# Performance work log

Measured on AMD Instinct MI355X. Metric: run time of the kernel, lower is better.

## Reference

```python
import jax, jax.numpy as jnp
import numpy as np

EPS = 1e-8  # torch CosineSimilarity default eps

def _normalize(x):
    # torch clamps each norm at eps before dividing
    n = jnp.sqrt(jnp.sum(x * x, axis=-1, keepdims=True))
    return x / jnp.maximum(n, EPS)

def _cross_entropy(logits, labels):
    logp = jax.nn.log_softmax(logits, axis=-1)
    return -jnp.mean(jnp.take_along_axis(logp, labels[:, None], axis=-1))

def setup_inputs() -> dict:
    key = jax.random.key(0)
    ks = jax.random.split(key, 7)
    B, M, D = 8192, 3129, 512
    return {
        'mm_proj': jax.random.normal(ks[0], (B, D), jnp.float32),
        'ans_embedding': jax.random.normal(ks[1], (M, D), jnp.float32),
        'v_max': jax.random.normal(ks[2], (B, D), jnp.float32),
        'mm': jax.random.normal(ks[3], (B, D), jnp.float32),
        'logits_q': jax.random.normal(ks[4], (B, M), jnp.float32),
        'logits_rubi': jax.random.normal(ks[5], (B, M), jnp.float32),
        'class_id': jax.random.randint(ks[6], (B, 1), 0, M, jnp.int64),
    }

def reference(mm_proj, ans_embedding, v_max, mm, logits_q, logits_rubi, class_id,
              question_loss_weight=1.0):
    cid = class_id.squeeze(1)  # [B]
    # NCE over cosine similarities: fuse normalize + GEMM instead of [B,M,D] expand
    g = _normalize(mm_proj)          # [B, D]
    a = _normalize(ans_embedding)    # [M, D]
    d_logit = jnp.einsum('bd,md->bm', g, a)  # [B, M] cosine matrix
    positive_dist = jnp.take_along_axis(d_logit, cid[:, None], axis=1)[:, 0]  # [B]
    num = jnp.exp(positive_dist)
    den = jnp.sum(jnp.exp(d_logit), axis=-1)
    loss_nce = jnp.mean(-jnp.log(num / den))
    # object cosine loss
    obj_dist = jnp.sum(_normalize(v_max) * _normalize(mm), axis=-1)  # [B]
    obj_loss = jnp.mean(1.0 - obj_dist)
    fusion_loss = (_cross_entropy(logits_rubi, cid) + obj_loss + loss_nce) / 3.0
    question_loss = _cross_entropy(logits_q, cid)
    loss = fusion_loss + question_loss_weight * question_loss
    # out['loss'], out['loss_mm_q'], out['loss_q']
    return jnp.stack([loss, fusion_loss, question_loss])
```

## Files before the change

### kernel.cpp

```cpp
#include <hip/hip_runtime.h>
#include <hip/hip_bf16.h>

#define B_N 8192
#define M_N 3129
#define M_PAD 3200
#define D_N 512

#define CE_L 12
#define CE_SPAN (CE_L * 256)
#define CE_WPA 8344
#define CE_WTOT (2 * CE_WPA)
#define CE_BLOCKS (CE_WTOT / 4)

#define PREP_G_BLOCKS   (B_N / 4)
#define PREP_A_BLOCKS   (M_PAD / 4)
#define PREP_OBJ_BLOCKS (B_N / 4)
#define ZERO_FLOATS (3 * B_N + 8)
#define ZERO_BLOCKS 25
#define A_BLOCKS (PREP_G_BLOCKS + PREP_A_BLOCKS + PREP_OBJ_BLOCKS + ZERO_BLOCKS)

#define GEMM_TILES ((M_PAD / 128) * (B_N / 128))
#define B_BLOCKS 8000
#define POS_BLOCKS_B (B_BLOCKS - GEMM_TILES - CE_BLOCKS)

#define GLOBAL_AS __attribute__((address_space(1)))
#define LDS_AS __attribute__((address_space(3)))

typedef __bf16 bf16x8 __attribute__((ext_vector_type(8)));
typedef float f32x4 __attribute__((ext_vector_type(4)));

__device__ __forceinline__ f32x4 nt_load4(const float* p) {
  return __builtin_nontemporal_load((const f32x4*)p);
}

__device__ __forceinline__ void ce_span(
    int gw, const float* __restrict__ lq, const float* __restrict__ lr,
    float* __restrict__ rowsum) {
  const int lane = threadIdx.x & 63;
  const int aidx = (gw >= CE_WPA) ? 1 : 0;
  const unsigned wl = (unsigned)(gw - aidx * CE_WPA);
  const unsigned f0 = wl * (unsigned)CE_SPAN;
  const unsigned r0 = f0 / (unsigned)M_N;
  const unsigned b1 = (r0 + 1u) * (unsigned)M_N;
  const float* base = aidx ? lr : lq;
  const float* p = base + f0 + (unsigned)lane * 4u;

  f32x4 buf[6];
#pragma unroll
  for (int i = 0; i < 6; ++i) buf[i] = nt_load4(p + i * 256);

  float a0 = 0.f, a1 = 0.f;
  const unsigned fbase = f0 + (unsigned)lane * 4u;
#pragma unroll
  for (int i = 0; i < CE_L; ++i) {
    f32x4 v = buf[i % 6];
    if (i + 6 < CE_L) buf[i % 6] = nt_load4(p + (i + 6) * 256);
    unsigned f = fbase + (unsigned)i * 256u;
    float e0 = __expf(v.x), e1 = __expf(v.y), e2 = __expf(v.z), e3 = __expf(v.w);
    float lo = 0.f, hi = 0.f;
    if (f + 0u < b1) lo += e0; else hi += e0;
    if (f + 1u < b1) lo += e1; else hi += e1;
    if (f + 2u < b1) lo += e2; else hi += e2;
    if (f + 3u < b1) lo += e3; else hi += e3;
    a0 += lo; a1 += hi;
  }
  for (int o = 1; o < 64; o <<= 1) {
    a0 += __shfl_xor(a0, o);
    a1 += __shfl_xor(a1, o);
  }
  if (lane == 0) {
    float* rs = rowsum + (aidx ? B_N : 0);
    atomicAdd(rs + r0, a0);
    if (a1 != 0.f) atomicAdd(rs + r0 + 1, a1);
  }
}

__device__ __forceinline__ void normalize_row(
    const float* __restrict__ x, __bf16* __restrict__ y,
    int row, int nrows_src, int lane) {
  bf16x8 out;
  if (row >= nrows_src) {
    for (int j = 0; j < 8; ++j) out[j] = (__bf16)0.0f;
    *(bf16x8*)(y + (size_t)row * D_N + lane * 8) = out;
    return;
  }
  const float* xr = x + (size_t)row * D_N + lane * 8;
  f32x4 v0 = *(const f32x4*)xr;
  f32x4 v1 = *(const f32x4*)(xr + 4);
  float s = v0.x*v0.x + v0.y*v0.y + v0.z*v0.z + v0.w*v0.w
          + v1.x*v1.x + v1.y*v1.y + v1.z*v1.z + v1.w*v1.w;
  for (int o = 1; o < 64; o <<= 1) s += __shfl_xor(s, o);
  float rn = 1.0f / fmaxf(sqrtf(s), 1e-8f);
  float vals[8] = {v0.x, v0.y, v0.z, v0.w, v1.x, v1.y, v1.z, v1.w};
  for (int j = 0; j < 8; ++j) out[j] = (__bf16)(vals[j] * rn);
  *(bf16x8*)(y + (size_t)row * D_N + lane * 8) = out;
}

__global__ __launch_bounds__(256) void a_prep_kernel(
    const float* __restrict__ mm_proj, const float* __restrict__ ans_emb,
    const float* __restrict__ v_max, const float* __restrict__ mm,
    __bf16* __restrict__ g, __bf16* __restrict__ a,
    float* __restrict__ obj, float* __restrict__ zbase) {
  int blk = blockIdx.x;
  int wid = threadIdx.x >> 6, lane = threadIdx.x & 63;
  if (blk < PREP_G_BLOCKS) {
    normalize_row(mm_proj, g, blk * 4 + wid, B_N, lane);
  } else if (blk < PREP_G_BLOCKS + PREP_A_BLOCKS) {
    normalize_row(ans_emb, a, (blk - PREP_G_BLOCKS) * 4 + wid, M_N, lane);
  } else if (blk < PREP_G_BLOCKS + PREP_A_BLOCKS + PREP_OBJ_BLOCKS) {
    int b = (blk - PREP_G_BLOCKS - PREP_A_BLOCKS) * 4 + wid;
    const float* vr = v_max + (size_t)b * D_N + lane * 8;
    const float* mr = mm + (size_t)b * D_N + lane * 8;
    f32x4 a0 = nt_load4(vr), a1 = nt_load4(vr + 4);
    f32x4 b0 = nt_load4(mr), b1 = nt_load4(mr + 4);
    float sv = a0.x*a0.x + a0.y*a0.y + a0.z*a0.z + a0.w*a0.w
             + a1.x*a1.x + a1.y*a1.y + a1.z*a1.z + a1.w*a1.w;
    float sm = b0.x*b0.x + b0.y*b0.y + b0.z*b0.z + b0.w*b0.w
             + b1.x*b1.x + b1.y*b1.y + b1.z*b1.z + b1.w*b1.w;
    float sd = a0.x*b0.x + a0.y*b0.y + a0.z*b0.z + a0.w*b0.w
             + a1.x*b1.x + a1.y*b1.y + a1.z*b1.z + a1.w*b1.w;
    for (int o = 1; o < 64; o <<= 1) {
      sv += __shfl_xor(sv, o);
      sm += __shfl_xor(sm, o);
      sd += __shfl_xor(sd, o);
    }
    if (lane == 0) {
      float dist = sd / (fmaxf(sqrtf(sv), 1e-8f) * fmaxf(sqrtf(sm), 1e-8f));
      obj[b] = 1.0f - dist;
    }
  } else {
    int zb = blk - (PREP_G_BLOCKS + PREP_A_BLOCKS + PREP_OBJ_BLOCKS);
    int idx = (zb * 256 + threadIdx.x) * 4;
    if (idx < ZERO_FLOATS) *(f32x4*)(zbase + idx) = f32x4{0.f, 0.f, 0.f, 0.f};
  }
}

__device__ __forceinline__ void gemm_stage(
    const __bf16* __restrict__ g, const __bf16* __restrict__ a,
    __bf16* As, __bf16* Bs, int t, int brow0, int mrow0, int k0) {
#pragma unroll
  for (int i = 0; i < 2; ++i) {
    int s = t + i * 256;
    int row = s >> 2;
    int kq = (s & 3) << 3;
    const __bf16* ga = g + (size_t)(brow0 + row) * D_N + (k0 + kq);
    __builtin_amdgcn_global_load_lds((const GLOBAL_AS void*)ga,
                                     (LDS_AS void*)(As + s * 8), 16, 0, 0);
    const __bf16* gb = a + (size_t)(mrow0 + row) * D_N + (k0 + kq);
    __builtin_amdgcn_global_load_lds((const GLOBAL_AS void*)gb,
                                     (LDS_AS void*)(Bs + s * 8), 16, 0, 0);
  }
}

__global__ __launch_bounds__(256) void b_fused_kernel(
    const __bf16* __restrict__ g, const __bf16* __restrict__ a,
    const int* __restrict__ cid,
    const float* __restrict__ mm_proj, const float* __restrict__ ans_emb,
    const float* __restrict__ lq, const float* __restrict__ lr,
    float* __restrict__ den, float* __restrict__ pos,
    float* __restrict__ rowsum) {
  __shared__ __bf16 As[2][128 * 32];
  __shared__ __bf16 Bs[2][128 * 32];
  const int t = threadIdx.x;
  const int lane = t & 63;
  const int wid = t >> 6;

  const int blk = blockIdx.x;
  const int mod = blk % 5;
  const int div5 = blk / 5;

  if (mod == 2) {
    const int tile = div5;
    const int brow0 = (tile / (M_PAD / 128)) * 128;
    const int mrow0 = (tile % (M_PAD / 128)) * 128;
    const int wrow = wid >> 1;
    const int wcol = wid & 1;
    const int r = lane & 15;
    const int quad = lane >> 4;

    f32x4 acc[4][4];
    for (int i = 0; i < 4; ++i)
      for (int j = 0; j < 4; ++j)
        acc[i][j] = f32x4{0.f, 0.f, 0.f, 0.f};

    gemm_stage(g, a, &As[0][0], &Bs[0][0], t, brow0, mrow0, 0);
    int cur = 0;
    __syncthreads();

    for (int ks = 0; ks < D_N / 32; ++ks) {
      if (ks + 1 < D_N / 32)
        gemm_stage(g, a, &As[cur ^ 1][0], &Bs[cur ^ 1][0], t, brow0, mrow0,
                   (ks + 1) * 32);
      bf16x8 af[4], bfr[4];
#pragma unroll
      for (int i = 0; i < 4; ++i)
        af[i] = *(const bf16x8*)(&As[cur][(wrow * 64 + i * 16 + r) * 32 + quad * 8]);
#pragma unroll
      for (int j = 0; j < 4; ++j)
        bfr[j] = *(const bf16x8*)(&Bs[cur][(wcol * 64 + j * 16 + r) * 32 + quad * 8]);
#pragma unroll
      for (int i = 0; i < 4; ++i)
#pragma unroll
        for (int j = 0; j < 4; ++j)
          acc[i][j] = __builtin_amdgcn_mfma_f32_16x16x32_bf16(af[i], bfr[j],
                                                              acc[i][j], 0, 0, 0);
      __syncthreads();
      cur ^= 1;
    }

    for (int i = 0; i < 4; ++i) {
      for (int reg = 0; reg < 4; ++reg) {
        float s = 0.0f;
        for (int j = 0; j < 4; ++j) {
          int m = mrow0 + wcol * 64 + j * 16 + r;
          if (m < M_N) s += __expf(acc[i][j][reg]);
        }
        s += __shfl_xor(s, 1);
        s += __shfl_xor(s, 2);
        s += __shfl_xor(s, 4);
        s += __shfl_xor(s, 8);
        if (r == 0) {
          int b = brow0 + wrow * 64 + i * 16 + quad * 4 + reg;
          atomicAdd(den + b, s);
        }
      }
    }
    return;
  }

  const int other = div5 * 4 + mod - (mod > 2 ? 1 : 0);
  if (other < CE_BLOCKS) {
    ce_span(other * 4 + wid, lq, lr, rowsum);
    return;
  }

  {
    int b = (other - CE_BLOCKS) * 4 + wid;
    if (b >= B_N) return;
    int label = cid[b];
    const float* xr = mm_proj + (size_t)b * D_N + lane * 8;
    f32x4 v0 = *(const f32x4*)xr, v1 = *(const f32x4*)(xr + 4);
    const float* yr = ans_emb + (size_t)label * D_N + lane * 8;
    f32x4 w0 = *(const f32x4*)yr, w1 = *(const f32x4*)(yr + 4);
    float sg = v0.x*v0.x + v0.y*v0.y + v0.z*v0.z + v0.w*v0.w
             + v1.x*v1.x + v1.y*v1.y + v1.z*v1.z + v1.w*v1.w;
    float sa = w0.x*w0.x + w0.y*w0.y + w0.z*w0.z + w0.w*w0.w
             + w1.x*w1.x + w1.y*w1.y + w1.z*w1.z + w1.w*w1.w;
    for (int o = 1; o < 64; o <<= 1) {
      sg += __shfl_xor(sg, o);
      sa += __shfl_xor(sa, o);
    }
    float rng = 1.0f / fmaxf(sqrtf(sg), 1e-8f);
    float rna = 1.0f / fmaxf(sqrtf(sa), 1e-8f);
    float gv[8] = {v0.x, v0.y, v0.z, v0.w, v1.x, v1.y, v1.z, v1.w};
    float av[8] = {w0.x, w0.y, w0.z, w0.w, w1.x, w1.y, w1.z, w1.w};
    float d = 0.0f;
    for (int j = 0; j < 8; ++j)
      d += (float)(__bf16)(gv[j] * rng) * (float)(__bf16)(av[j] * rna);
    for (int o = 1; o < 64; o <<= 1) d += __shfl_xor(d, o);
    if (lane == 0) pos[b] = d;
  }
}

__global__ __launch_bounds__(256) void c_final_kernel(
    const float* __restrict__ den, const float* __restrict__ pos,
    const float* __restrict__ rowsum,
    const float* __restrict__ lq, const float* __restrict__ lr,
    const int* __restrict__ cid, const float* __restrict__ obj,
    float* __restrict__ acc, float* __restrict__ out) {
  int b = blockIdx.x * 256 + threadIdx.x;
  int lab = cid[b];
  float xq = lq[(size_t)b * M_N + lab];
  float xr = lr[(size_t)b * M_N + lab];
  float s_nce = logf(den[b]) - pos[b];
  float s_ceq = logf(rowsum[b]) - xq;
  float s_cer = logf(rowsum[B_N + b]) - xr;
  float s_obj = obj[b];
  for (int o = 1; o < 64; o <<= 1) {
    s_nce += __shfl_xor(s_nce, o);
    s_ceq += __shfl_xor(s_ceq, o);
    s_cer += __shfl_xor(s_cer, o);
    s_obj += __shfl_xor(s_obj, o);
  }
  __shared__ float red[4][4];
  int wid = threadIdx.x >> 6;
  if ((threadIdx.x & 63) == 0) {
    red[wid][0] = s_nce; red[wid][1] = s_ceq;
    red[wid][2] = s_cer; red[wid][3] = s_obj;
  }
  __syncthreads();
  if (threadIdx.x < 4) {
    float v = red[0][threadIdx.x] + red[1][threadIdx.x]
            + red[2][threadIdx.x] + red[3][threadIdx.x];
    atomicAdd(acc + threadIdx.x, v);
  }
  if (threadIdx.x == 0) {
    __threadfence();
    unsigned prev = atomicAdd((unsigned*)(acc + 4), 1u);
    if (prev == 31u) {
      float nce = atomicAdd(acc + 0, 0.0f) / (float)B_N;
      float ceq = atomicAdd(acc + 1, 0.0f) / (float)B_N;
      float cer = atomicAdd(acc + 2, 0.0f) / (float)B_N;
      float ob  = atomicAdd(acc + 3, 0.0f) / (float)B_N;
      float fusion = (cer + ob + nce) * (1.0f / 3.0f);
      out[0] = fusion + ceq;
      out[1] = fusion;
      out[2] = ceq;
    }
  }
}

extern "C" void kernel_launch(void* const* d_in, const int* in_sizes, int n_in,
                              void* d_out, int out_size, void* d_ws, size_t ws_size,
                              hipStream_t stream) {
  const float* mm_proj     = (const float*)d_in[0];
  const float* ans_emb     = (const float*)d_in[1];
  const float* v_max       = (const float*)d_in[2];
  const float* mm          = (const float*)d_in[3];
  const float* logits_q    = (const float*)d_in[4];
  const float* logits_rubi = (const float*)d_in[5];
  const int*   cid         = (const int*)d_in[6];
  float* out = (float*)d_out;

  char* ws = (char*)d_ws;
  __bf16* g = (__bf16*)ws;
  __bf16* a = (__bf16*)(ws + 8388608);
  float* den    = (float*)(ws + 8388608 + 3276800);
  float* rowsum = den + B_N;
  float* acc    = rowsum + 2 * B_N;
  float* pos    = acc + 8;
  float* obj    = pos + B_N;

  a_prep_kernel<<<A_BLOCKS, 256, 0, stream>>>(
      mm_proj, ans_emb, v_max, mm, g, a, obj, den);
  b_fused_kernel<<<B_BLOCKS, 256, 0, stream>>>(
      g, a, cid, mm_proj, ans_emb, logits_q, logits_rubi, den, pos, rowsum);
  c_final_kernel<<<B_N / 256, 256, 0, stream>>>(
      den, pos, rowsum, logits_q, logits_rubi, cid, obj, acc, out);
}
```

Before: 296.0 us.

## Triple-buffer GEMM LDS with single barrier per step and 1:1 block interleave

The GEMM k-loop moves from double to triple buffering with global_load_lds prefetch two stages ahead. It uses explicit vmcnt waits and one barrier per iteration instead of a full __syncthreads after compute. The block schedule also changes from a 1-in-5 GEMM interleave to alternating GEMM and CE/positive blocks for the first 2*GEMM_TILES blocks, with the rest following. This aims to hide global-load latency and spread GEMM tiles evenly alongside memory-bound CE work. The cost is more LDS per block, which may lower occupancy.

```diff
diff --git a/kernel.cpp b/kernel.cpp
--- a/kernel.cpp
+++ b/kernel.cpp
@@ -20,8 +20,9 @@
 #define A_BLOCKS (PREP_G_BLOCKS + PREP_A_BLOCKS + PREP_OBJ_BLOCKS + ZERO_BLOCKS)
 
 #define GEMM_TILES ((M_PAD / 128) * (B_N / 128))
+#define GEMM_REGION (2 * GEMM_TILES)
 #define B_BLOCKS 8000
-#define POS_BLOCKS_B (B_BLOCKS - GEMM_TILES - CE_BLOCKS)
+#define POS_BLOCKS (B_N / 4)
 
 #define GLOBAL_AS __attribute__((address_space(1)))
 #define LDS_AS __attribute__((address_space(3)))
@@ -159,84 +160,97 @@
     const float* __restrict__ lq, const float* __restrict__ lr,
     float* __restrict__ den, float* __restrict__ pos,
     float* __restrict__ rowsum) {
-  __shared__ __bf16 As[2][128 * 32];
-  __shared__ __bf16 Bs[2][128 * 32];
+  __shared__ __bf16 As[3][128 * 32];
+  __shared__ __bf16 Bs[3][128 * 32];
   const int t = threadIdx.x;
   const int lane = t & 63;
   const int wid = t >> 6;
-
   const int blk = blockIdx.x;
-  const int mod = blk % 5;
-  const int div5 = blk / 5;
-
-  if (mod == 2) {
-    const int tile = div5;
-    const int brow0 = (tile / (M_PAD / 128)) * 128;
-    const int mrow0 = (tile % (M_PAD / 128)) * 128;
-    const int wrow = wid >> 1;
-    const int wcol = wid & 1;
-    const int r = lane & 15;
-    const int quad = lane >> 4;
-
-    f32x4 acc[4][4];
-    for (int i = 0; i < 4; ++i)
-      for (int j = 0; j < 4; ++j)
-        acc[i][j] = f32x4{0.f, 0.f, 0.f, 0.f};
-
-    gemm_stage(g, a, &As[0][0], &Bs[0][0], t, brow0, mrow0, 0);
-    int cur = 0;
-    __syncthreads();
-
-    for (int ks = 0; ks < D_N / 32; ++ks) {
-      if (ks + 1 < D_N / 32)
-        gemm_stage(g, a, &As[cur ^ 1][0], &Bs[cur ^ 1][0], t, brow0, mrow0,
-                   (ks + 1) * 32);
-      bf16x8 af[4], bfr[4];
-#pragma unroll
+
+  int other;
+  if (blk < GEMM_REGION) {
+    if (blk & 1) {
+      const int tile = blk >> 1;
+      const int brow0 = (tile / (M_PAD / 128)) * 128;
+      const int mrow0 = (tile % (M_PAD / 128)) * 128;
+      const int wrow = wid >> 1;
+      const int wcol = wid & 1;
+      const int r = lane & 15;
+      const int quad = lane >> 4;
+
+      f32x4 acc[4][4];
       for (int i = 0; i < 4; ++i)
-        af[i] = *(const bf16x8*)(&As[cur][(wrow * 64 + i * 16 + r) * 32 + quad * 8]);
-#pragma unroll
-      for (int j = 0; j < 4; ++j)
-        bfr[j] = *(const bf16x8*)(&Bs[cur][(wcol * 64 + j * 16 + r) * 32 + quad * 8]);
-#pragma unroll
-      for (int i = 0; i < 4; ++i)
-#pragma unroll
         for (int j = 0; j < 4; ++j)
-          acc[i][j] = __builtin_amdgcn_mfma_f32_16x16x32_bf16(af[i], bfr[j],
-                                                              acc[i][j], 0, 0, 0);
-      __syncthreads();
-      cur ^= 1;
-    }
-
-    for (int i = 0; i < 4; ++i) {
-      for (int reg = 0; reg < 4; ++reg) {
-        float s = 0.0f;
-        for (int j = 0; j < 4; ++j) {
-          int m = mrow0 + wcol * 64 + j * 16 + r;
-          if (m < M_N) s += __expf(acc[i][j][reg]);
+          acc[i][j] = f32x4{0.f, 0.f, 0.f, 0.f};
+
+      gemm_stage(g, a, &As[0][0], &Bs[0][0], t, brow0, mrow0, 0);
+      gemm_stage(g, a, &As[1][0], &Bs[1][0], t, brow0, mrow0, 32);
+      asm volatile("s_waitcnt vmcnt(4)" ::: "memory");
+      __builtin_amdgcn_s_barrier();
+      __builtin_amdgcn_sched_barrier(0);
+
+#pragma unroll
+      for (int ks = 0; ks < 16; ++ks) {
+        if (ks < 14)
+          gemm_stage(g, a, &As[(ks + 2) % 3][0], &Bs[(ks + 2) % 3][0], t,
+                     brow0, mrow0, (ks + 2) * 32);
+        const __bf16* Ab = &As[ks % 3][0];
+        const __bf16* Bb = &Bs[ks % 3][0];
+        bf16x8 af[4], bfr[4];
+#pragma unroll
+        for (int i = 0; i < 4; ++i)
+          af[i] = *(const bf16x8*)(Ab + (wrow * 64 + i * 16 + r) * 32 + quad * 8);
+#pragma unroll
+        for (int j = 0; j < 4; ++j)
+          bfr[j] = *(const bf16x8*)(Bb + (wcol * 64 + j * 16 + r) * 32 + quad * 8);
+#pragma unroll
+        for (int i = 0; i < 4; ++i)
+#pragma unroll
+          for (int j = 0; j < 4; ++j)
+            acc[i][j] = __builtin_amdgcn_mfma_f32_16x16x32_bf16(af[i], bfr[j],
+                                                                acc[i][j], 0, 0, 0);
+        if (ks < 14) {
+          asm volatile("s_waitcnt vmcnt(4)" ::: "memory");
+        } else if (ks == 14) {
+          asm volatile("s_waitcnt vmcnt(0)" ::: "memory");
         }
-        s += __shfl_xor(s, 1);
-        s += __shfl_xor(s, 2);
-        s += __shfl_xor(s, 4);
-        s += __shfl_xor(s, 8);
-        if (r == 0) {
-          int b = brow0 + wrow * 64 + i * 16 + quad * 4 + reg;
-          atomicAdd(den + b, s);
+        if (ks < 15) {
+          __builtin_amdgcn_s_barrier();
+          __builtin_amdgcn_sched_barrier(0);
         }
       }
-    }
-    return;
-  }
-
-  const int other = div5 * 4 + mod - (mod > 2 ? 1 : 0);
+
+      for (int i = 0; i < 4; ++i) {
+        for (int reg = 0; reg < 4; ++reg) {
+          float s = 0.0f;
+          for (int j = 0; j < 4; ++j) {
+            int m = mrow0 + wcol * 64 + j * 16 + r;
+            if (m < M_N) s += __expf(acc[i][j][reg]);
+          }
+          s += __shfl_xor(s, 1);
+          s += __shfl_xor(s, 2);
+          s += __shfl_xor(s, 4);
+          s += __shfl_xor(s, 8);
+          if (r == 0) {
+            int b = brow0 + wrow * 64 + i * 16 + quad * 4 + reg;
+            atomicAdd(den + b, s);
+          }
+        }
+      }
+      return;
+    }
+    other = blk >> 1;
+  } else {
+    other = GEMM_TILES + (blk - GEMM_REGION);
+  }
+
   if (other < CE_BLOCKS) {
     ce_span(other * 4 + wid, lq, lr, rowsum);
     return;
   }
-
-  {
-    int b = (other - CE_BLOCKS) * 4 + wid;
-    if (b >= B_N) return;
+  other -= CE_BLOCKS;
+  if (other < POS_BLOCKS) {
+    int b = other * 4 + wid;
     int label = cid[b];
     const float* xr = mm_proj + (size_t)b * D_N + lane * 8;
     f32x4 v0 = *(const f32x4*)xr, v1 = *(const f32x4*)(xr + 4);
```

Result: slower. 312.3 us (+5.5%).

## Fold final reduction into fused kernel via last-block pattern; single-buffer GEMM LDS

Applied to the files above, without the earlier changes.

Removes the separate final kernel by having every block of the fused kernel bump a completion counter, with the last block reading den/pos/rowsum and the label logits to produce the three losses. The GEMM path also drops LDS double buffering in favour of a single buffer with barriers before and after each stage, which halves LDS per block and may raise occupancy but loses load/compute overlap. The change saves one launch and its dependency gap, but the final reduction now runs serially in one block of 256 threads over 8192 rows.

```diff
diff --git a/kernel.cpp b/kernel.cpp
--- a/kernel.cpp
+++ b/kernel.cpp
@@ -21,7 +21,7 @@
 
 #define GEMM_TILES ((M_PAD / 128) * (B_N / 128))
 #define B_BLOCKS 8000
-#define POS_BLOCKS_B (B_BLOCKS - GEMM_TILES - CE_BLOCKS)
+#define POS_BLOCKS (B_N / 4)
 
 #define GLOBAL_AS __attribute__((address_space(1)))
 #define LDS_AS __attribute__((address_space(3)))
@@ -158,19 +158,21 @@
     const float* __restrict__ mm_proj, const float* __restrict__ ans_emb,
     const float* __restrict__ lq, const float* __restrict__ lr,
     float* __restrict__ den, float* __restrict__ pos,
-    float* __restrict__ rowsum) {
-  __shared__ __bf16 As[2][128 * 32];
-  __shared__ __bf16 Bs[2][128 * 32];
+    float* __restrict__ rowsum, const float* __restrict__ obj,
+    float* __restrict__ acc, float* __restrict__ out) {
+  __shared__ __bf16 As[128 * 32];
+  __shared__ __bf16 Bs[128 * 32];
+  __shared__ float fred[4][4];
+  __shared__ unsigned s_last;
   const int t = threadIdx.x;
   const int lane = t & 63;
   const int wid = t >> 6;
-
   const int blk = blockIdx.x;
   const int mod = blk % 5;
-  const int div5 = blk / 5;
+  const int d5 = blk / 5;
 
   if (mod == 2) {
-    const int tile = div5;
+    const int tile = d5;
     const int brow0 = (tile / (M_PAD / 128)) * 128;
     const int mrow0 = (tile % (M_PAD / 128)) * 128;
     const int wrow = wid >> 1;
@@ -178,34 +180,28 @@
     const int r = lane & 15;
     const int quad = lane >> 4;
 
-    f32x4 acc[4][4];
+    f32x4 acc_r[4][4];
     for (int i = 0; i < 4; ++i)
       for (int j = 0; j < 4; ++j)
-        acc[i][j] = f32x4{0.f, 0.f, 0.f, 0.f};
-
-    gemm_stage(g, a, &As[0][0], &Bs[0][0], t, brow0, mrow0, 0);
-    int cur = 0;
-    __syncthreads();
-
-    for (int ks = 0; ks < D_N / 32; ++ks) {
-      if (ks + 1 < D_N / 32)
-        gemm_stage(g, a, &As[cur ^ 1][0], &Bs[cur ^ 1][0], t, brow0, mrow0,
-                   (ks + 1) * 32);
+        acc_r[i][j] = f32x4{0.f, 0.f, 0.f, 0.f};
+
+    for (int k0 = 0; k0 < D_N; k0 += 32) {
+      __syncthreads();
+      gemm_stage(g, a, As, Bs, t, brow0, mrow0, k0);
+      __syncthreads();
       bf16x8 af[4], bfr[4];
 #pragma unroll
       for (int i = 0; i < 4; ++i)
-        af[i] = *(const bf16x8*)(&As[cur][(wrow * 64 + i * 16 + r) * 32 + quad * 8]);
+        af[i] = *(const bf16x8*)(As + (wrow * 64 + i * 16 + r) * 32 + quad * 8);
 #pragma unroll
       for (int j = 0; j < 4; ++j)
-        bfr[j] = *(const bf16x8*)(&Bs[cur][(wcol * 64 + j * 16 + r) * 32 + quad * 8]);
+        bfr[j] = *(const bf16x8*)(Bs + (wcol * 64 + j * 16 + r) * 32 + quad * 8);
 #pragma unroll
       for (int i = 0; i < 4; ++i)
 #pragma unroll
         for (int j = 0; j < 4; ++j)
-          acc[i][j] = __builtin_amdgcn_mfma_f32_16x16x32_bf16(af[i], bfr[j],
-                                                              acc[i][j], 0, 0, 0);
-      __syncthreads();
-      cur ^= 1;
+          acc_r[i][j] = __builtin_amdgcn_mfma_f32_16x16x32_bf16(
+              af[i], bfr[j], acc_r[i][j], 0, 0, 0);
     }
 
     for (int i = 0; i < 4; ++i) {
@@ -213,7 +209,7 @@
         float s = 0.0f;
         for (int j = 0; j < 4; ++j) {
           int m = mrow0 + wcol * 64 + j * 16 + r;
-          if (m < M_N) s += __expf(acc[i][j][reg]);
+          if (m < M_N) s += __expf(acc_r[i][j][reg]);
         }
         s += __shfl_xor(s, 1);
         s += __shfl_xor(s, 2);
@@ -225,88 +221,82 @@
         }
       }
     }
-    return;
-  }
-
-  const int other = div5 * 4 + mod - (mod > 2 ? 1 : 0);
-  if (other < CE_BLOCKS) {
-    ce_span(other * 4 + wid, lq, lr, rowsum);
-    return;
-  }
-
-  {
-    int b = (other - CE_BLOCKS) * 4 + wid;
-    if (b >= B_N) return;
-    int label = cid[b];
-    const float* xr = mm_proj + (size_t)b * D_N + lane * 8;
-    f32x4 v0 = *(const f32x4*)xr, v1 = *(const f32x4*)(xr + 4);
-    const float* yr = ans_emb + (size_t)label * D_N + lane * 8;
-    f32x4 w0 = *(const f32x4*)yr, w1 = *(const f32x4*)(yr + 4);
-    float sg = v0.x*v0.x + v0.y*v0.y + v0.z*v0.z + v0.w*v0.w
-             + v1.x*v1.x + v1.y*v1.y + v1.z*v1.z + v1.w*v1.w;
-    float sa = w0.x*w0.x + w0.y*w0.y + w0.z*w0.z + w0.w*w0.w
-             + w1.x*w1.x + w1.y*w1.y + w1.z*w1.z + w1.w*w1.w;
-    for (int o = 1; o < 64; o <<= 1) {
-      sg += __shfl_xor(sg, o);
-      sa += __shfl_xor(sa, o);
-    }
-    float rng = 1.0f / fmaxf(sqrtf(sg), 1e-8f);
-    float rna = 1.0f / fmaxf(sqrtf(sa), 1e-8f);
-    float gv[8] = {v0.x, v0.y, v0.z, v0.w, v1.x, v1.y, v1.z, v1.w};
-    float av[8] = {w0.x, w0.y, w0.z, w0.w, w1.x, w1.y, w1.z, w1.w};
-    float d = 0.0f;
-    for (int j = 0; j < 8; ++j)
-      d += (float)(__bf16)(gv[j] * rng) * (float)(__bf16)(av[j] * rna);
-    for (int o = 1; o < 64; o <<= 1) d += __shfl_xor(d, o);
-    if (lane == 0) pos[b] = d;
-  }
-}
-
-__global__ __launch_bounds__(256) void c_final_kernel(
-    const float* __restrict__ den, const float* __restrict__ pos,
-    const float* __restrict__ rowsum,
-    const float* __restrict__ lq, const float* __restrict__ lr,
-    const int* __restrict__ cid, const float* __restrict__ obj,
-    float* __restrict__ acc, float* __restrict__ out) {
-  int b = blockIdx.x * 256 + threadIdx.x;
-  int lab = cid[b];
-  float xq = lq[(size_t)b * M_N + lab];
-  float xr = lr[(size_t)b * M_N + lab];
-  float s_nce = logf(den[b]) - pos[b];
-  float s_ceq = logf(rowsum[b]) - xq;
-  float s_cer = logf(rowsum[B_N + b]) - xr;
-  float s_obj = obj[b];
+  } else {
+    const int other = d5 * 4 + mod - (mod > 2 ? 1 : 0);
+    if (other < CE_BLOCKS) {
+      ce_span(other * 4 + wid, lq, lr, rowsum);
+    } else if (other - CE_BLOCKS < POS_BLOCKS) {
+      int b = (other - CE_BLOCKS) * 4 + wid;
+      int label = cid[b];
+      const float* xr = mm_proj + (size_t)b * D_N + lane * 8;
+      f32x4 v0 = *(const f32x4*)xr, v1 = *(const f32x4*)(xr + 4);
+      const float* yr = ans_emb + (size_t)label * D_N + lane * 8;
+      f32x4 w0 = *(const f32x4*)yr, w1 = *(const f32x4*)(yr + 4);
+      float sg = v0.x*v0.x + v0.y*v0.y + v0.z*v0.z + v0.w*v0.w
+               + v1.x*v1.x + v1.y*v1.y + v1.z*v1.z + v1.w*v1.w;
+      float sa = w0.x*w0.x + w0.y*w0.y + w0.z*w0.z + w0.w*w0.w
+               + w1.x*w1.x + w1.y*w1.y + w1.z*w1.z + w1.w*w1.w;
+      for (int o = 1; o < 64; o <<= 1) {
+        sg += __shfl_xor(sg, o);
+        sa += __shfl_xor(sa, o);
+      }
+      float rng = 1.0f / fmaxf(sqrtf(sg), 1e-8f);
+      float rna = 1.0f / fmaxf(sqrtf(sa), 1e-8f);
+      float gv[8] = {v0.x, v0.y, v0.z, v0.w, v1.x, v1.y, v1.z, v1.w};
+      float av[8] = {w0.x, w0.y, w0.z, w0.w, w1.x, w1.y, w1.z, w1.w};
+      float d = 0.0f;
+      for (int j = 0; j < 8; ++j)
+        d += (float)(__bf16)(gv[j] * rng) * (float)(__bf16)(av[j] * rna);
+      for (int o = 1; o < 64; o <<= 1) d += __shfl_xor(d, o);
+      if (lane == 0) pos[b] = d;
+    }
+  }
+
+  __syncthreads();
+  if (t == 0) {
+    __threadfence();
+    s_last = (atomicAdd((unsigned*)(acc + 4), 1u) == (unsigned)(B_BLOCKS - 1));
+  }
+  __syncthreads();
+  if (!s_last) return;
+  __threadfence();
+
+  float s_nce = 0.f, s_ceq = 0.f, s_cer = 0.f, s_obj = 0.f;
+#pragma unroll 4
+  for (int jj = 0; jj < 32; ++jj) {
+    int b = jj * 256 + t;
+    int lab = cid[b];
+    float xq = lq[(size_t)b * M_N + lab];
+    float xr = lr[(size_t)b * M_N + lab];
+    float dn = atomicAdd(den + b, 0.0f);
+    float ps = atomicAdd(pos + b, 0.0f);
+    float rq = atomicAdd(rowsum + b, 0.0f);
+    float rr = atomicAdd(rowsum + B_N + b, 0.0f);
+    s_nce += logf(dn) - ps;
+    s_ceq += logf(rq) - xq;
+    s_cer += logf(rr) - xr;
+    s_obj += obj[b];
+  }
   for (int o = 1; o < 64; o <<= 1) {
     s_nce += __shfl_xor(s_nce, o);
     s_ceq += __shfl_xor(s_ceq, o);
     s_cer += __shfl_xor(s_cer, o);
     s_obj += __shfl_xor(s_obj, o);
   }
-  __shared__ float red[4][4];
-  int wid = threadIdx.x >> 6;
-  if ((threadIdx.x & 63) == 0) {
-    red[wid][0] = s_nce; red[wid][1] = s_ceq;
-    red[wid][2] = s_cer; red[wid][3] = s_obj;
+  if (lane == 0) {
+    fred[wid][0] = s_nce; fred[wid][1] = s_ceq;
+    fred[wid][2] = s_cer; fred[wid][3] = s_obj;
   }
   __syncthreads();
-  if (threadIdx.x < 4) {
-    float v = red[0][threadIdx.x] + red[1][threadIdx.x]
-            + red[2][threadIdx.x] + red[3][threadIdx.x];
-    atomicAdd(acc + threadIdx.x, v);
-  }
-  if (threadIdx.x == 0) {
-    __threadfence();
-    unsigned prev = atomicAdd((unsigned*)(acc + 4), 1u);
-    if (prev == 31u) {
-      float nce = atomicAdd(acc + 0, 0.0f) / (float)B_N;
-      float ceq = atomicAdd(acc + 1, 0.0f) / (float)B_N;
-      float cer = atomicAdd(acc + 2, 0.0f) / (float)B_N;
-      float ob  = atomicAdd(acc + 3, 0.0f) / (float)B_N;
-      float fusion = (cer + ob + nce) * (1.0f / 3.0f);
-      out[0] = fusion + ceq;
-      out[1] = fusion;
-      out[2] = ceq;
-    }
+  if (t == 0) {
+    float nce = (fred[0][0] + fred[1][0] + fred[2][0] + fred[3][0]) / (float)B_N;
+    float ceq = (fred[0][1] + fred[1][1] + fred[2][1] + fred[3][1]) / (float)B_N;
+    float cer = (fred[0][2] + fred[1][2] + fred[2][2] + fred[3][2]) / (float)B_N;
+    float ob  = (fred[0][3] + fred[1][3] + fred[2][3] + fred[3][3]) / (float)B_N;
+    float fusion = (cer + ob + nce) * (1.0f / 3.0f);
+    out[0] = fusion + ceq;
+    out[1] = fusion;
+    out[2] = ceq;
   }
 }
 
@@ -334,7 +324,6 @@
   a_prep_kernel<<<A_BLOCKS, 256, 0, stream>>>(
       mm_proj, ans_emb, v_max, mm, g, a, obj, den);
   b_fused_kernel<<<B_BLOCKS, 256, 0, stream>>>(
-      g, a, cid, mm_proj, ans_emb, logits_q, logits_rubi, den, pos, rowsum);
-  c_final_kernel<<<B_N / 256, 256, 0, stream>>>(
-      den, pos, rowsum, logits_q, logits_rubi, cid, obj, acc, out);
-}
+      g, a, cid, mm_proj, ans_emb, logits_q, logits_rubi, den, pos, rowsum,
+      obj, acc, out);
+}
```

Measured after the change: 669.8 us. 2.26x slower.
